# Kernel optimization log

Measured on AMD Instinct MI355X. Metric: run time of the kernel, lower is better.

Reference implementation:

```python
import jax, jax.numpy as jnp
import numpy as np

N, D_IN, D_EMB, K = 16384, 1024, 256, 1024
ALPHA, EPS = 0.01, 1e-5


def setup_inputs() -> dict:
    key = jax.random.key(0)
    ks = jax.random.split(key, 6)
    inp = jax.random.normal(ks[0], (N, D_IN), dtype=jnp.float32)
    W_send = jax.random.normal(ks[1], (D_IN, D_EMB), dtype=jnp.float32) / np.sqrt(D_IN)
    b_send = jnp.zeros((D_EMB,), dtype=jnp.float32)
    W_recv = jax.random.normal(ks[2], (D_EMB, D_IN), dtype=jnp.float32) / np.sqrt(D_EMB)
    b_recv = jnp.zeros((D_IN,), dtype=jnp.float32)
    codebook = jax.random.normal(ks[3], (K, D_EMB), dtype=jnp.float32)
    ema_vecs = codebook.copy()
    ema_size = jnp.zeros((K,), dtype=jnp.float32)
    return {"input": inp, "W_send": W_send, "b_send": b_send,
            "W_recv": W_recv, "b_recv": b_recv, "codebook": codebook,
            "ema_vecs": ema_vecs, "ema_size": ema_size}


def reference(input, W_send, b_send, W_recv, b_recv, codebook, ema_vecs, ema_size):
    sg = jax.lax.stop_gradient
    # send projection -> latent z  [N, D_EMB]
    z = input @ W_send + b_send
    # nearest-neighbor lookup: argmin_k ||e_k||^2 - 2 <z, e_k>
    sqr = jnp.sum(codebook * codebook, axis=1)          # [K]
    cov = jnp.einsum('nj,kj->nk', z, codebook)          # [N, K]
    codes = jnp.argmin(sqr - 2.0 * cov, axis=-1)        # [N] int
    # fetch embeddings (gather)
    vectors = codebook[codes]                            # [N, D_EMB]
    # mse losses, reduction='sum'
    embedding = jnp.sum((vectors - sg(z)) ** 2)
    commitment = jnp.sum((z - sg(vectors)) ** 2)
    # straight-through output
    emb_out = z + sg(vectors - z)
    # EMA accumulate (one-hot scatter == segment_sum)
    upd_vecs = jax.ops.segment_sum(z, codes, num_segments=K)              # [K, D_EMB]
    upd_size = jax.ops.segment_sum(jnp.ones((z.shape[0],), z.dtype), codes, num_segments=K)
    ema_vecs_new = ema_vecs + ALPHA * (upd_vecs - ema_vecs)
    ema_size_new = ema_size + ALPHA * (upd_size - ema_size)
    # EMA update (Laplace-smoothed centroid)
    n = jnp.sum(ema_size_new)
    coef = n / (n + K * EPS)
    size = coef * (ema_size_new + EPS)
    weight_new = ema_vecs_new / size[:, None]
    # empirical entropy of the codes in bits
    prob = jnp.bincount(codes, length=K).astype(jnp.float32) / codes.size
    ent = -jnp.sum(jnp.where(prob > 0, prob * jnp.log(prob), 0.0)) / jnp.log(2.0)
    # recv projection
    x = emb_out @ W_recv + b_recv
    return (x, codes, embedding, commitment, ent, ema_vecs_new, ema_size_new, weight_new)
```

## Files before the change

kernel.cpp:

```cpp
#include <hip/hip_runtime.h>
#include <math.h>

#define NROWS 16384
#define DIN   1024
#define DEMB  256
#define KC    1024
#define ALPHA 0.01f
#define EPSV  1e-5f
#define INV2048 4.8828125e-4f
#define CHUNK 32
#define COV_CHUNKS 8

typedef _Float16 f16;
typedef __attribute__((ext_vector_type(4)))  _Float16 f16x4;
typedef __attribute__((ext_vector_type(8)))  _Float16 f16x8;
typedef __attribute__((ext_vector_type(16))) float    f32x16;
typedef unsigned long long u64;

#define OFF_Z       0
#define OFF_R       4194304
#define OFF_SQR     5242880
#define OFF_ZH      5243904
#define OFF_ZL      7341056
#define OFF_WTH     9438208
#define OFF_WTL     9569280
#define OFF_CBH     9700352
#define OFF_CBL     9831424
#define OFF_KEYS    9962496
#define OFF_CODES   9995264
#define OFF_LIST    10011648
#define OFF_OFFS    10028032
#define OFF_UPD     10029056
#define OFF_HIST    10291200
#define OFF_CURSOR  10292224
#define OFF_LOSS    10293248
#define OFF_SIZE    10294288

#define OUT_X      0
#define OUT_CODES  16777216
#define OUT_EMB    16793600
#define OUT_COMMIT 16793601
#define OUT_ENT    16793602
#define OUT_EMAV   16793603
#define OUT_EMAS   17055747
#define OUT_W      17056771

__device__ __forceinline__ void split_f32(float x, f16& h, f16& l) {
    h = (f16)x;
    l = (f16)((x - (float)h) * 2048.0f);
}

__global__ __launch_bounds__(256) void prep_kernel(const float* __restrict__ W_send,
                                                   const float* __restrict__ W_recv,
                                                   const float* __restrict__ cb,
                                                   float* __restrict__ ws) {
    const int b = blockIdx.x;
    const int t = threadIdx.x;
    int* wsi = (int*)ws;

    if (b < 256) {
        f16* wth = (f16*)(ws + OFF_WTH);
        f16* wtl = (f16*)(ws + OFF_WTL);
        const int n = b;
        f16x4 h4, l4;
#pragma unroll
        for (int j = 0; j < 4; ++j) {
            int k = t * 4 + j;
            float x = W_send[(size_t)k * DEMB + n];
            f16 h, l; split_f32(x, h, l);
            h4[j] = h; l4[j] = l;
        }
        *(f16x4*)&wth[(size_t)n * DIN + t * 4] = h4;
        *(f16x4*)&wtl[(size_t)n * DIN + t * 4] = l4;
    } else if (b < 512) {
        f16* cbh = (f16*)(ws + OFF_CBH);
        f16* cbl = (f16*)(ws + OFF_CBL);
        int idx = ((b - 256) * 256 + t) * 4;
        float4 v = *(const float4*)&cb[idx];
        f16x4 h4, l4;
        f16 h, l;
        split_f32(v.x, h, l); h4[0] = h; l4[0] = l;
        split_f32(v.y, h, l); h4[1] = h; l4[1] = l;
        split_f32(v.z, h, l); h4[2] = h; l4[2] = l;
        split_f32(v.w, h, l); h4[3] = h; l4[3] = l;
        *(f16x4*)&cbh[idx] = h4;
        *(f16x4*)&cbl[idx] = l4;
    } else if (b < 768) {
        f16* wrh = (f16*)(ws + OFF_ZH);
        f16* wrl = (f16*)(ws + OFF_ZH + 131072);
        const int n = (b - 512) * 4 + (t >> 6);
        const int lane = t & 63;
        f16x4 h4, l4;
#pragma unroll
        for (int j = 0; j < 4; ++j) {
            int k = lane * 4 + j;
            float x = W_recv[(size_t)k * DIN + n];
            f16 h, l; split_f32(x, h, l);
            h4[j] = h; l4[j] = l;
        }
        *(f16x4*)&wrh[(size_t)n * DEMB + lane * 4] = h4;
        *(f16x4*)&wrl[(size_t)n * DEMB + lane * 4] = l4;
    } else if (b < 1024) {
        float* sqr = ws + OFF_SQR;
        const int k = (b - 768) * 4 + (t >> 6);
        const int lane = t & 63;
        float4 v = ((const float4*)cb)[k * 64 + lane];
        float s = v.x * v.x + v.y * v.y + v.z * v.z + v.w * v.w;
        for (int off = 32; off > 0; off >>= 1) s += __shfl_down(s, off, 64);
        if (lane == 0) sqr[k] = s;
    } else if (b < 1280) {
        float4 zed = make_float4(0.f, 0.f, 0.f, 0.f);
        *(float4*)&ws[OFF_UPD + (size_t)(b - 1024) * 1024 + t * 4] = zed;
    } else if (b == 1280) {
#pragma unroll
        for (int j = 0; j < 4; ++j) {
            wsi[OFF_HIST + t * 4 + j] = 0;
            wsi[OFF_CURSOR + t * 4 + j] = 0;
        }
        if (t < 16) ws[OFF_LOSS + t] = 0.f;
    } else if (b < 1345) {
        u64* keys = (u64*)(ws + OFF_KEYS);
        keys[(b - 1281) * 256 + t] = ~0ull;
    } else {
        float4 zed = make_float4(0.f, 0.f, 0.f, 0.f);
        *(float4*)&ws[OFF_R + (size_t)(b - 1345) * 1024 + t * 4] = zed;
    }
}

__global__ __launch_bounds__(512) void gemm1_mfma(const float* __restrict__ in,
                                                  const f16* __restrict__ wth,
                                                  const f16* __restrict__ wtl,
                                                  const float* __restrict__ bsend,
                                                  float* __restrict__ z,
                                                  f16* __restrict__ zh,
                                                  f16* __restrict__ zl) {
    __shared__ f16 sm[2 * 2 * 2 * 128 * 64];
    const int tid = threadIdx.x;
    const int wave = tid >> 6, lane = tid & 63;
    const int half = lane >> 5, l31 = lane & 31;
    const int wrow = wave >> 2, wcol = wave & 3;

    const int L = blockIdx.x;
    const int v = L >> 3;
    const int bx = v & 1;
    const int by = (L & 7) + 8 * (v >> 1);
    const int rowBase = by * 128;
    const int colBase = bx * 128;

    const int sr  = tid >> 2;
    const int skq = tid & 3;
    const int sr7 = sr & 7;

    f32x16 accm[2] = {};
    f32x16 accx[2] = {};

    auto stageB = [&](int buf, int ks) {
#pragma unroll
        for (int i = 0; i < 4; ++i) {
            const int q  = wave * 4 + i;
            const int hl = q >> 4;
            const int c  = (q & 15) * 8 + (lane >> 3);
            const int p  = lane & 7;
            const int s  = p ^ (c & 7);
            const f16* src = (hl ? wtl : wth)
                           + (size_t)(colBase + c) * DIN + ks + s * 8;
            f16* dst = sm + buf * 32768 + 16384 + q * 512 + lane * 8;
            __builtin_amdgcn_global_load_lds(
                (const __attribute__((address_space(1))) void*)src,
                (__attribute__((address_space(3))) void*)dst, 16, 0, 0);
        }
    };

    auto loadA = [&](int ks, float4* av) {
        const float* src = &in[(size_t)(rowBase + sr) * DIN + ks + skq * 16];
#pragma unroll
        for (int j = 0; j < 4; ++j) av[j] = ((const float4*)src)[j];
    };

    auto writeA = [&](int buf, const float4* av) {
        f16* Abase = sm + buf * 32768;
#pragma unroll
        for (int q = 0; q < 2; ++q) {
            f16x8 h8, l8;
#pragma unroll
            for (int j = 0; j < 2; ++j) {
                float4 v4 = av[q * 2 + j];
                f16 h, l;
                split_f32(v4.x, h, l); h8[j * 4 + 0] = h; l8[j * 4 + 0] = l;
                split_f32(v4.y, h, l); h8[j * 4 + 1] = h; l8[j * 4 + 1] = l;
                split_f32(v4.z, h, l); h8[j * 4 + 2] = h; l8[j * 4 + 2] = l;
                split_f32(v4.w, h, l); h8[j * 4 + 3] = h; l8[j * 4 + 3] = l;
            }
            const int s = skq * 2 + q;
            const int off = sr * 64 + ((s ^ sr7) << 3);
            *(f16x8*)&Abase[off] = h8;
            *(f16x8*)&Abase[8192 + off] = l8;
        }
    };

    auto compute = [&](int buf) {
        const f16* Ah = sm + buf * 32768;
        const f16* Al = Ah + 8192;
        const f16* Bh = Ah + 16384;
        const f16* Bl = Ah + 24576;
        const int c  = wcol * 32 + l31;
        const int c7 = c & 7;
#pragma unroll
        for (int t4 = 0; t4 < 4; ++t4) {
            const int s = t4 * 2 + half;
            f16x8 a_h[2], a_l[2];
#pragma unroll
            for (int rt = 0; rt < 2; ++rt) {
                const int r = wrow * 64 + rt * 32 + l31;
                const int off = r * 64 + ((s ^ (r & 7)) << 3);
                a_h[rt] = *(const f16x8*)&Ah[off];
                a_l[rt] = *(const f16x8*)&Al[off];
            }
            const int boff = c * 64 + ((s ^ c7) << 3);
            f16x8 b_h = *(const f16x8*)&Bh[boff];
            f16x8 b_l = *(const f16x8*)&Bl[boff];
#pragma unroll
            for (int rt = 0; rt < 2; ++rt) {
                accm[rt] = __builtin_amdgcn_mfma_f32_32x32x16_f16(a_h[rt], b_h, accm[rt], 0, 0, 0);
                accx[rt] = __builtin_amdgcn_mfma_f32_32x32x16_f16(a_h[rt], b_l, accx[rt], 0, 0, 0);
                accx[rt] = __builtin_amdgcn_mfma_f32_32x32x16_f16(a_l[rt], b_h, accx[rt], 0, 0, 0);
            }
        }
    };

    stageB(0, 0);
    {
        float4 av[4];
        loadA(0, av);
        writeA(0, av);
    }
    __syncthreads();

    int cur = 0;
    for (int step = 0; step < 16; ++step) {
        float4 av[4];
        const bool pf = (step + 1) < 16;
        if (pf) {
            stageB(cur ^ 1, (step + 1) * 64);
            loadA((step + 1) * 64, av);
        }
        compute(cur);
        if (pf) writeA(cur ^ 1, av);
        __syncthreads();
        cur ^= 1;
    }

#pragma unroll
    for (int rt = 0; rt < 2; ++rt) {
        const int col = colBase + wcol * 32 + l31;
        const float bb = bsend[col];
#pragma unroll
        for (int reg = 0; reg < 16; ++reg) {
            const int row = rowBase + wrow * 64 + rt * 32 + (reg & 3) + 8 * (reg >> 2) + 4 * half;
            const float zv = accm[rt][reg] + INV2048 * accx[rt][reg] + bb;
            const size_t o = (size_t)row * DEMB + col;
            z[o] = zv;
            f16 h = (f16)zv;
            zh[o] = h;
            zl[o] = (f16)((zv - (float)h) * 2048.0f);
        }
    }
}

__global__ __launch_bounds__(256, 2) void gemm2_mfma(const f16* __restrict__ cbh,
                                                     const f16* __restrict__ cbl,
                                                     const f16* __restrict__ wrh,
                                                     const f16* __restrict__ wrl,
                                                     float* __restrict__ R) {
    __shared__ f16 sm[2 * 16384];
    const int tid = threadIdx.x;
    const int wave = tid >> 6, lane = tid & 63;
    const int half = lane >> 5, l31 = lane & 31;
    const int wr = wave >> 1, wc = wave & 1;

    const int L = blockIdx.x;
    const int kz = L & 1;
    const int tile = L >> 1;
    const int rowBase = (tile >> 4) * 64;
    const int colBase = (tile & 15) * 64;
    const int ks0 = kz * 128;

    f32x16 accm = {}, accx = {};

    auto stage = [&](int buf, int ks) {
#pragma unroll
        for (int i = 0; i < 8; ++i) {
            const int q   = wave * 8 + i;
            const int arr = q >> 3;
            const int grp = q & 7;
            const int r   = grp * 8 + (lane >> 3);
            const int p   = lane & 7;
            const int s   = p ^ (r & 7);
            const f16* basep = (arr == 0) ? cbh : (arr == 1) ? cbl
                             : (arr == 2) ? wrh : wrl;
            const int rowg = ((arr >= 2) ? colBase : rowBase) + r;
            const f16* src = basep + (size_t)rowg * DEMB + ks + s * 8;
            f16* dst = sm + buf * 16384 + arr * 4096 + grp * 512;
            __builtin_amdgcn_global_load_lds(
                (const __attribute__((address_space(1))) void*)src,
                (__attribute__((address_space(3))) void*)dst, 16, 0, 0);
        }
    };

    stage(0, ks0);
    for (int s = 0; s < 2; ++s) {
        __syncthreads();
        if (s == 0) stage(1, ks0 + 64);
        const f16* base = sm + s * 16384;
#pragma unroll
        for (int t = 0; t < 4; ++t) {
            const int sgi = t * 2 + half;
            const int ar = wr * 32 + l31;
            const int bc = wc * 32 + l31;
            const int aoff = ar * 64 + ((sgi ^ (ar & 7)) << 3);
            const int boff = bc * 64 + ((sgi ^ (bc & 7)) << 3);
            f16x8 a_h = *(const f16x8*)&base[aoff];
            f16x8 a_l = *(const f16x8*)&base[4096 + aoff];
            f16x8 b_h = *(const f16x8*)&base[8192 + boff];
            f16x8 b_l = *(const f16x8*)&base[12288 + boff];
            accm = __builtin_amdgcn_mfma_f32_32x32x16_f16(a_h, b_h, accm, 0, 0, 0);
            accx = __builtin_amdgcn_mfma_f32_32x32x16_f16(a_h, b_l, accx, 0, 0, 0);
            accx = __builtin_amdgcn_mfma_f32_32x32x16_f16(a_l, b_h, accx, 0, 0, 0);
        }
    }

    const int col = colBase + wc * 32 + l31;
#pragma unroll
    for (int reg = 0; reg < 16; ++reg) {
        const int row = rowBase + wr * 32 + (reg & 3) + 8 * (reg >> 2) + 4 * half;
        atomicAdd(&R[(size_t)row * DIN + col], accm[reg] + INV2048 * accx[reg]);
    }
}

__device__ __forceinline__ void cov_stage(const f16* __restrict__ cbh,
                                          const f16* __restrict__ cbl,
                                          f16* sC, int buf, int codeBase,
                                          int wave, int lane) {
#pragma unroll
    for (int i = 0; i < 8; ++i) {
        const int seg = wave * 8 + i;
        const int hl  = seg >> 4;
        const int rp  = seg & 15;
        const int r   = rp * 2 + (lane >> 5);
        const f16* src = (hl ? cbl : cbh)
                       + (size_t)(codeBase + r) * DEMB
                       + (((lane & 31) ^ r) << 3);
        f16* dst = sC + (((buf << 1) + hl) * 32 + rp * 2) * DEMB;
        __builtin_amdgcn_global_load_lds(
            (const __attribute__((address_space(1))) void*)src,
            (__attribute__((address_space(3))) void*)dst,
            16, 0, 0);
    }
}

__global__ __launch_bounds__(256, 2) void cov_mfma_kernel(const f16* __restrict__ zh,
                                                          const f16* __restrict__ zl,
                                                          const f16* __restrict__ cbh,
                                                          const f16* __restrict__ cbl,
                                                          const float* __restrict__ sqr,
                                                          u64* __restrict__ keys) {
    __shared__ f16 sC[2 * 2 * 32 * DEMB];
    const int tid = threadIdx.x;
    const int wave = tid >> 6, lane = tid & 63;
    const int half = lane >> 5, l31 = lane & 31;

    const int L = blockIdx.x;
    const int v = L >> 3;
    const int bx = v & 3;
    const int by = (L & 7) + 8 * (v >> 2);

    const int rowBase = by * 128 + wave * 32;
    const int myRow = rowBase + l31;
    const int cb0 = bx * (COV_CHUNKS * 32);

    cov_stage(cbh, cbl, sC, 0, cb0, wave, lane);

    f16x8 a_h[16], a_l[16];
#pragma unroll
    for (int t = 0; t < 16; ++t) {
        size_t o = (size_t)myRow * DEMB + t * 16 + half * 8;
        a_h[t] = *(const f16x8*)&zh[o];
        a_l[t] = *(const f16x8*)&zl[o];
    }

    float runv[16];
    int   runc[16];
#pragma unroll
    for (int r = 0; r < 16; ++r) { runv[r] = 3.4e38f; runc[r] = 0; }

    for (int cc = 0; cc < COV_CHUNKS; ++cc) {
        __syncthreads();
        if (cc + 1 < COV_CHUNKS)
            cov_stage(cbh, cbl, sC, (cc + 1) & 1, cb0 + (cc + 1) * 32, wave, lane);

        const f16* Ch = sC + ((cc & 1) * 2 + 0) * 32 * DEMB;
        const f16* Cl = sC + ((cc & 1) * 2 + 1) * 32 * DEMB;

        f32x16 accm = {};
        f32x16 accx = {};
#pragma unroll
        for (int t = 0; t < 16; ++t) {
            const int seg = t * 2 + half;
            const int p = ((seg ^ l31) << 3);
            f16x8 b_h = *(const f16x8*)&Ch[l31 * DEMB + p];
            f16x8 b_l = *(const f16x8*)&Cl[l31 * DEMB + p];
            accm = __builtin_amdgcn_mfma_f32_32x32x16_f16(a_h[t], b_h, accm, 0, 0, 0);
            accx = __builtin_amdgcn_mfma_f32_32x32x16_f16(a_h[t], b_l, accx, 0, 0, 0);
            accx = __builtin_amdgcn_mfma_f32_32x32x16_f16(a_l[t], b_h, accx, 0, 0, 0);
        }

        const int code = cb0 + cc * 32 + l31;
        const float sqv = sqr[code];
#pragma unroll
        for (int r = 0; r < 16; ++r) {
            float s = sqv - 2.0f * (accm[r] + INV2048 * accx[r]);
            if (s < runv[r]) { runv[r] = s; runc[r] = code; }
        }
    }

#pragma unroll
    for (int r = 0; r < 16; ++r) {
        float v2 = runv[r]; int ci = runc[r];
        for (int off = 16; off > 0; off >>= 1) {
            float ov = __shfl_down(v2, off, 32);
            int   oc = __shfl_down(ci, off, 32);
            if (ov < v2 || (ov == v2 && oc < ci)) { v2 = ov; ci = oc; }
        }
        if (l31 == 0) {
            int row = rowBase + (r & 3) + 8 * (r >> 2) + 4 * half;
            unsigned ub = __float_as_uint(v2);
            ub = (ub & 0x80000000u) ? ~ub : (ub | 0x80000000u);
            u64 key = ((u64)ub << 32) | (unsigned)ci;
            atomicMin(&keys[row], key);
        }
    }
}

__global__ __launch_bounds__(256) void decode_kernel(const u64* __restrict__ keys,
                                                     int* __restrict__ codes,
                                                     float* __restrict__ out_codes,
                                                     int* __restrict__ hist) {
    int r = blockIdx.x * 256 + threadIdx.x;
    int c = (int)(keys[r] & 0xFFFFFFFFull);
    codes[r] = c;
    out_codes[r] = (float)c;
    atomicAdd(&hist[c], 1);
}

__global__ __launch_bounds__(1024) void prefix_kernel(const int* __restrict__ hist,
                                                      const float* __restrict__ ema_size,
                                                      int* __restrict__ offs,
                                                      float* __restrict__ size_ws,
                                                      float* __restrict__ out) {
    __shared__ int s[1024];
    __shared__ float rn[1024];
    __shared__ float re[1024];
    const int t = threadIdx.x;
    const int v = hist[t];
    s[t] = v;
    const float c = (float)v;
    const float es = ema_size[t];
    const float esn = es + ALPHA * (c - es);
    out[OUT_EMAS + t] = esn;
    const float p = c * (1.0f / (float)NROWS);
    rn[t] = esn;
    re[t] = (p > 0.f) ? p * logf(p) : 0.f;
    __syncthreads();
    for (int d = 1; d < 1024; d <<= 1) {
        int x = (t >= d) ? s[t - d] : 0;
        __syncthreads();
        s[t] += x;
        __syncthreads();
    }
    offs[t] = s[t] - v;
    for (int d = 512; d > 0; d >>= 1) {
        if (t < d) { rn[t] += rn[t + d]; re[t] += re[t + d]; }
        __syncthreads();
    }
    const float n = rn[0];
    const float coef = n / (n + (float)KC * EPSV);
    size_ws[t] = coef * (esn + EPSV);
    if (t == 0) out[OUT_ENT] = -re[0] / logf(2.0f);
}

__global__ __launch_bounds__(256) void fill_kernel(const int* __restrict__ codes,
                                                   const int* __restrict__ offs,
                                                   int* __restrict__ cursor,
                                                   int* __restrict__ list) {
    int r = blockIdx.x * 256 + threadIdx.x;
    int c = codes[r];
    int pos = offs[c] + atomicAdd(&cursor[c], 1);
    list[pos] = r;
}

__global__ __launch_bounds__(256) void upd_loss_kernel(const float* __restrict__ z,
                                                       const float* __restrict__ cb,
                                                       const int* __restrict__ list,
                                                       const int* __restrict__ codes,
                                                       float* __restrict__ upd,
                                                       float* __restrict__ loss,
                                                       float* __restrict__ out_losses) {
    __shared__ int srow[CHUNK];
    __shared__ int scode[CHUNK];
    const int tid = threadIdx.x;
    const int base = blockIdx.x * CHUNK;
    if (tid < CHUNK) {
        int r = list[base + tid];
        srow[tid] = r;
        scode[tid] = codes[r];
    }
    __syncthreads();

    int cur = scode[0];
    float cbv = cb[(size_t)cur * DEMB + tid];
    float acc = 0.f, lacc = 0.f;
    float zv = z[(size_t)srow[0] * DEMB + tid];
#pragma unroll 4
    for (int i = 0; i < CHUNK; ++i) {
        float znext = (i + 1 < CHUNK) ? z[(size_t)srow[i + 1] * DEMB + tid] : 0.f;
        int c = scode[i];
        if (c != cur) {
            atomicAdd(&upd[(size_t)cur * DEMB + tid], acc);
            acc = 0.f;
            cur = c;
            cbv = cb[(size_t)cur * DEMB + tid];
        }
        acc += zv;
        float d = zv - cbv;
        lacc += d * d;
        zv = znext;
    }
    atomicAdd(&upd[(size_t)cur * DEMB + tid], acc);

    __shared__ float red[256];
    red[tid] = lacc;
    __syncthreads();
    for (int s = 128; s > 0; s >>= 1) {
        if (tid < s) red[tid] += red[tid + s];
        __syncthreads();
    }
    if (tid == 0) {
        atomicAdd(loss, red[0]);
        __threadfence();
        int tk = atomicAdd((int*)(loss + 8), 1);
        if (tk == (int)gridDim.x - 1) {
            float l = atomicAdd(loss, 0.0f);
            out_losses[0] = l;
            out_losses[1] = l;
        }
    }
}

__global__ __launch_bounds__(256) void tail_kernel(const float* __restrict__ R,
                                                   const float* __restrict__ brecv,
                                                   const int* __restrict__ codes,
                                                   const float* __restrict__ ema_vecs,
                                                   const float* __restrict__ upd,
                                                   const float* __restrict__ size_ws,
                                                   float* __restrict__ out) {
    const int b = blockIdx.x;
    const int t = threadIdx.x;
    if (b < NROWS) {
        const int code = codes[b];
        float4 r = ((const float4*)(R + (size_t)code * DIN))[t];
        float4 bb = ((const float4*)brecv)[t];
        ((float4*)(out + OUT_X + (size_t)b * DIN))[t] =
            make_float4(r.x + bb.x, r.y + bb.y, r.z + bb.z, r.w + bb.w);
    } else {
        const int idx = (b - NROWS) * 256 + t;
        float ev = ema_vecs[idx], uv = upd[idx];
        float evn = ev + ALPHA * (uv - ev);
        out[OUT_EMAV + idx] = evn;
        out[OUT_W + idx] = evn / size_ws[idx >> 8];
    }
}

extern "C" void kernel_launch(void* const* d_in, const int* in_sizes, int n_in,
                              void* d_out, int out_size, void* d_ws, size_t ws_size,
                              hipStream_t stream) {
    const float* input    = (const float*)d_in[0];
    const float* W_send   = (const float*)d_in[1];
    const float* b_send   = (const float*)d_in[2];
    const float* W_recv   = (const float*)d_in[3];
    const float* b_recv   = (const float*)d_in[4];
    const float* codebook = (const float*)d_in[5];
    const float* ema_vecs = (const float*)d_in[6];
    const float* ema_size = (const float*)d_in[7];
    float* out = (float*)d_out;
    float* ws  = (float*)d_ws;
    int*   wsi = (int*)d_ws;

    f16* wth = (f16*)(ws + OFF_WTH);
    f16* wtl = (f16*)(ws + OFF_WTL);
    f16* cbh = (f16*)(ws + OFF_CBH);
    f16* cbl = (f16*)(ws + OFF_CBL);
    f16* zh  = (f16*)(ws + OFF_ZH);
    f16* zl  = (f16*)(ws + OFF_ZL);
    u64* keys = (u64*)(ws + OFF_KEYS);
    f16* wrh = (f16*)(ws + OFF_ZH);
    f16* wrl = (f16*)(ws + OFF_ZH + 131072);

    prep_kernel<<<2369, 256, 0, stream>>>(W_send, W_recv, codebook, ws);

    gemm2_mfma<<<512, 256, 0, stream>>>(
        cbh, cbl, wrh, wrl, ws + OFF_R);

    gemm1_mfma<<<(DEMB / 128) * (NROWS / 128), 512, 0, stream>>>(
        input, wth, wtl, b_send, ws + OFF_Z, zh, zl);

    cov_mfma_kernel<<<(KC / (COV_CHUNKS * 32)) * (NROWS / 128), 256, 0, stream>>>(
        zh, zl, cbh, cbl, ws + OFF_SQR, keys);

    decode_kernel<<<NROWS / 256, 256, 0, stream>>>(
        keys, wsi + OFF_CODES, out + OUT_CODES, wsi + OFF_HIST);

    prefix_kernel<<<1, 1024, 0, stream>>>(
        wsi + OFF_HIST, ema_size, wsi + OFF_OFFS, ws + OFF_SIZE, out);

    fill_kernel<<<NROWS / 256, 256, 0, stream>>>(
        wsi + OFF_CODES, wsi + OFF_OFFS, wsi + OFF_CURSOR, wsi + OFF_LIST);

    upd_loss_kernel<<<NROWS / CHUNK, 256, 0, stream>>>(
        ws + OFF_Z, codebook, wsi + OFF_LIST, wsi + OFF_CODES,
        ws + OFF_UPD, ws + OFF_LOSS, out + OUT_EMB);

    tail_kernel<<<NROWS + 1024, 256, 0, stream>>>(
        ws + OFF_R, b_recv, wsi + OFF_CODES, ema_vecs,
        ws + OFF_UPD, ws + OFF_SIZE, out);
}
```

Measured before the change: 264.2 us.

## Drop fp32 z buffer and split cov kernel over more code blocks

gemm1 no longer writes fp32 z. upd_loss now rebuilds z from the fp16 hi/lo pair, which removes a 16 MB write and a later fp32 read. The cov kernel now splits the codebook into 8 slices of 128 codes instead of 4 of 256, doubling the grid. It also switches to a single-buffered LDS stage with explicit syncs, which halves shared memory but loses load/compute overlap. Reconstructing z from the hi/lo pair may introduce tiny precision differences in the loss and update values.

```diff
diff --git a/kernel.cpp b/kernel.cpp
--- a/kernel.cpp
+++ b/kernel.cpp
@@ -131,7 +131,6 @@
                                                   const f16* __restrict__ wth,
                                                   const f16* __restrict__ wtl,
                                                   const float* __restrict__ bsend,
-                                                  float* __restrict__ z,
                                                   f16* __restrict__ zh,
                                                   f16* __restrict__ zl) {
     __shared__ f16 sm[2 * 2 * 2 * 128 * 64];
@@ -259,7 +258,6 @@
             const int row = rowBase + wrow * 64 + rt * 32 + (reg & 3) + 8 * (reg >> 2) + 4 * half;
             const float zv = accm[rt][reg] + INV2048 * accx[rt][reg] + bb;
             const size_t o = (size_t)row * DEMB + col;
-            z[o] = zv;
             f16 h = (f16)zv;
             zh[o] = h;
             zl[o] = (f16)((zv - (float)h) * 2048.0f);
@@ -339,7 +337,7 @@
 
 __device__ __forceinline__ void cov_stage(const f16* __restrict__ cbh,
                                           const f16* __restrict__ cbl,
-                                          f16* sC, int buf, int codeBase,
+                                          f16* sC, int codeBase,
                                           int wave, int lane) {
 #pragma unroll
     for (int i = 0; i < 8; ++i) {
@@ -350,7 +348,7 @@
         const f16* src = (hl ? cbl : cbh)
                        + (size_t)(codeBase + r) * DEMB
                        + (((lane & 31) ^ r) << 3);
-        f16* dst = sC + (((buf << 1) + hl) * 32 + rp * 2) * DEMB;
+        f16* dst = sC + (hl * 32 + rp * 2) * DEMB;
         __builtin_amdgcn_global_load_lds(
             (const __attribute__((address_space(1))) void*)src,
             (__attribute__((address_space(3))) void*)dst,
@@ -364,21 +362,19 @@
                                                           const f16* __restrict__ cbl,
                                                           const float* __restrict__ sqr,
                                                           u64* __restrict__ keys) {
-    __shared__ f16 sC[2 * 2 * 32 * DEMB];
+    __shared__ f16 sC[2 * 32 * DEMB];
     const int tid = threadIdx.x;
     const int wave = tid >> 6, lane = tid & 63;
     const int half = lane >> 5, l31 = lane & 31;
 
     const int L = blockIdx.x;
     const int v = L >> 3;
-    const int bx = v & 3;
-    const int by = (L & 7) + 8 * (v >> 2);
+    const int bx = v & 7;
+    const int by = (L & 7) + 8 * (v >> 3);
 
     const int rowBase = by * 128 + wave * 32;
     const int myRow = rowBase + l31;
-    const int cb0 = bx * (COV_CHUNKS * 32);
-
-    cov_stage(cbh, cbl, sC, 0, cb0, wave, lane);
+    const int cb0 = bx * 128;
 
     f16x8 a_h[16], a_l[16];
 #pragma unroll
@@ -393,13 +389,12 @@
 #pragma unroll
     for (int r = 0; r < 16; ++r) { runv[r] = 3.4e38f; runc[r] = 0; }
 
-    for (int cc = 0; cc < COV_CHUNKS; ++cc) {
-        __syncthreads();
-        if (cc + 1 < COV_CHUNKS)
-            cov_stage(cbh, cbl, sC, (cc + 1) & 1, cb0 + (cc + 1) * 32, wave, lane);
-
-        const f16* Ch = sC + ((cc & 1) * 2 + 0) * 32 * DEMB;
-        const f16* Cl = sC + ((cc & 1) * 2 + 1) * 32 * DEMB;
+    for (int cc = 0; cc < 4; ++cc) {
+        cov_stage(cbh, cbl, sC, cb0 + cc * 32, wave, lane);
+        __syncthreads();
+
+        const f16* Ch = sC;
+        const f16* Cl = sC + 32 * DEMB;
 
         f32x16 accm = {};
         f32x16 accx = {};
@@ -421,6 +416,7 @@
             float s = sqv - 2.0f * (accm[r] + INV2048 * accx[r]);
             if (s < runv[r]) { runv[r] = s; runc[r] = code; }
         }
+        __syncthreads();
     }
 
 #pragma unroll
@@ -498,7 +494,8 @@
     list[pos] = r;
 }
 
-__global__ __launch_bounds__(256) void upd_loss_kernel(const float* __restrict__ z,
+__global__ __launch_bounds__(256) void upd_loss_kernel(const f16* __restrict__ zh,
+                                                       const f16* __restrict__ zl,
                                                        const float* __restrict__ cb,
                                                        const int* __restrict__ list,
                                                        const int* __restrict__ codes,
@@ -516,13 +513,18 @@
     }
     __syncthreads();
 
+    auto zread = [&](int row) {
+        size_t o = (size_t)row * DEMB + tid;
+        return (float)zh[o] + INV2048 * (float)zl[o];
+    };
+
     int cur = scode[0];
     float cbv = cb[(size_t)cur * DEMB + tid];
     float acc = 0.f, lacc = 0.f;
-    float zv = z[(size_t)srow[0] * DEMB + tid];
+    float zv = zread(srow[0]);
 #pragma unroll 4
     for (int i = 0; i < CHUNK; ++i) {
-        float znext = (i + 1 < CHUNK) ? z[(size_t)srow[i + 1] * DEMB + tid] : 0.f;
+        float znext = (i + 1 < CHUNK) ? zread(srow[i + 1]) : 0.f;
         int c = scode[i];
         if (c != cur) {
             atomicAdd(&upd[(size_t)cur * DEMB + tid], acc);
@@ -611,9 +613,9 @@
         cbh, cbl, wrh, wrl, ws + OFF_R);
 
     gemm1_mfma<<<(DEMB / 128) * (NROWS / 128), 512, 0, stream>>>(
-        input, wth, wtl, b_send, ws + OFF_Z, zh, zl);
-
-    cov_mfma_kernel<<<(KC / (COV_CHUNKS * 32)) * (NROWS / 128), 256, 0, stream>>>(
+        input, wth, wtl, b_send, zh, zl);
+
+    cov_mfma_kernel<<<8 * (NROWS / 128), 256, 0, stream>>>(
         zh, zl, cbh, cbl, ws + OFF_SQR, keys);
 
     decode_kernel<<<NROWS / 256, 256, 0, stream>>>(
@@ -626,7 +628,7 @@
         wsi + OFF_CODES, wsi + OFF_OFFS, wsi + OFF_CURSOR, wsi + OFF_LIST);
 
     upd_loss_kernel<<<NROWS / CHUNK, 256, 0, stream>>>(
-        ws + OFF_Z, codebook, wsi + OFF_LIST, wsi + OFF_CODES,
+        zh, zl, codebook, wsi + OFF_LIST, wsi + OFF_CODES,
         ws + OFF_UPD, ws + OFF_LOSS, out + OUT_EMB);
 
     tail_kernel<<<NROWS + 1024, 256, 0, stream>>>(
```

Result: slower. 270.6 us (+2.5%).
